# Optimization experiments

Measured on AMD Instinct MI355X. Metric: run time of the kernel, lower is better.

## Reference

```python
import jax, jax.numpy as jnp
import numpy as np

B = 200
SIZES = [65536, 16384, 4096, 1024, 256, 64]
DEG = 9
LOG_SIGMA = -1000.0  # weight log-sigma init (-1000) -> sigma = exp(-1000) == 0 in fp32, deterministic sample w = mu
P_DROP = 0.1
BN_EPS = 1e-5


def setup_inputs() -> dict:
    key = jax.random.key(0)
    ks = iter(jax.random.split(key, 64))
    d = {"x": jax.random.normal(next(ks), (B, SIZES[0], 3), jnp.float32)}
    din = 3
    for l in range(5):
        nin, nout = SIZES[l], SIZES[l + 1]
        E = nout * DEG
        d[f"src{l+1}"] = jax.random.randint(next(ks), (E,), 0, nin, dtype=jnp.int32)
        d[f"dst{l+1}"] = jnp.sort(jax.random.randint(next(ks), (E,), 0, nout, dtype=jnp.int32))
        d[f"w{l+1}"] = 0.1 * jax.random.normal(next(ks), (E, din, 1), jnp.float32)
        d[f"b{l+1}"] = 0.01 * jax.random.normal(next(ks), (nout, 1), jnp.float32)
        if l < 4:
            d[f"gamma{l+1}"] = jnp.ones((nout,), jnp.float32)
            d[f"beta{l+1}"] = jnp.zeros((nout,), jnp.float32)
        din = 1
    return d


def _pool(h, src, dst, w_mu, bias, n_out):
    # Bayesian sparse pooler: w = mu + exp(LOG_SIGMA)*eps == mu (sigma underflows to 0 in fp32)
    msgs = jnp.einsum('bed,edo->beo', h[:, src], w_mu)  # (B, E, dout) gathered weighted messages
    out = jnp.zeros((h.shape[0], n_out, w_mu.shape[2]), h.dtype).at[:, dst].add(msgs) + bias
    kl = jnp.sum(0.5 * (w_mu * w_mu - 1.0) - LOG_SIGMA)  # KL(N(mu, sig^2) || N(0, 1)) per weight, summed
    return out, kl


def _bn(h, gamma, beta):
    # training-mode BatchNorm1d over (B, C, 1): batch stats per channel (biased var, as torch)
    m = h.mean(axis=0, keepdims=True)
    v = h.var(axis=0, keepdims=True)
    hn = (h - m) * jax.lax.rsqrt(v + BN_EPS)
    return hn * gamma[None, :, None] + beta[None, :, None]


def _dropout(h, k):
    keep = jax.random.bernoulli(k, 1.0 - P_DROP, h.shape)
    return jnp.where(keep, h / (1.0 - P_DROP), jnp.zeros((), h.dtype))


def reference(x, src1, dst1, w1, b1, gamma1, beta1, src2, dst2, w2, b2, gamma2, beta2, src3, dst3, w3, b3, gamma3, beta3, src4, dst4, w4, b4, gamma4, beta4, src5, dst5, w5, b5):
    dkeys = jax.random.split(jax.random.key(42), 4)
    layers = [
        (src1, dst1, w1, b1, gamma1, beta1),
        (src2, dst2, w2, b2, gamma2, beta2),
        (src3, dst3, w3, b3, gamma3, beta3),
        (src4, dst4, w4, b4, gamma4, beta4),
    ]
    h = x
    kl_tot = jnp.float32(0.0)
    for l, (s, dd, w, b, g, bt) in enumerate(layers):
        h, kl = _pool(h, s, dd, w, b, SIZES[l + 1])
        kl_tot = kl_tot + kl
        h = _dropout(jax.nn.relu(_bn(h, g, bt)), dkeys[l])
    h, kl = _pool(h, src5, dst5, w5, b5, SIZES[5])
    kl_tot = kl_tot + kl
    return h[..., 0], kl_tot  # (B, 64), scalar KL
```

## Files before the change

kernel.cpp:

```cpp
#include <hip/hip_runtime.h>
#include <hip/hip_fp16.h>
#include <stdint.h>

#define B_    200
#define N0    65536
#define COLS  (N0 * 3)
#define JT    64
#define TPAD2 228

__device__ static inline unsigned short f2h(float f) {
  __half h = __float2half(f);
  return *reinterpret_cast<unsigned short*>(&h);
}
__device__ static inline float h2f(unsigned short u) {
  __half h = *reinterpret_cast<__half*>(&u);
  return __half2float(h);
}

__host__ __device__ static inline void tf2x32(uint32_t k0, uint32_t k1,
                                              uint32_t x0, uint32_t x1,
                                              uint32_t& o0, uint32_t& o1) {
  const uint32_t ks2 = k0 ^ k1 ^ 0x1BD11BDAu;
  x0 += k0; x1 += k1;
#define TF_R(r) { x0 += x1; x1 = (x1 << (r)) | (x1 >> (32 - (r))); x1 ^= x0; }
  TF_R(13) TF_R(15) TF_R(26) TF_R(6)   x0 += k1;  x1 += ks2 + 1u;
  TF_R(17) TF_R(29) TF_R(16) TF_R(24)  x0 += ks2; x1 += k0  + 2u;
  TF_R(13) TF_R(15) TF_R(26) TF_R(6)   x0 += k0;  x1 += k1  + 3u;
  TF_R(17) TF_R(29) TF_R(16) TF_R(24)  x0 += k1;  x1 += ks2 + 4u;
  TF_R(13) TF_R(15) TF_R(26) TF_R(6)   x0 += ks2; x1 += k0  + 5u;
#undef TF_R
  o0 = x0; o1 = x1;
}

__device__ static inline float drop_mask_apply(float hn, uint32_t b, uint32_t c,
                                               uint32_t nout, uint32_t k0, uint32_t k1) {
  uint32_t o0, o1;
  tf2x32(k0, k1, 0u, b * nout + c, o0, o1);
  uint32_t bits = o0 ^ o1;
  float u = __uint_as_float((bits >> 9) | 0x3f800000u) - 1.0f;
  return (u < 0.9f) ? hn * (1.0f / 0.9f) : 0.0f;
}

__global__ void build_rp_all(const int* __restrict__ dst0, const int* __restrict__ dst1,
                             const int* __restrict__ dst2, const int* __restrict__ dst3,
                             const int* __restrict__ dst4,
                             int* rp0, int* rp1, int* rp2, int* rp3, int* rp4,
                             float* kl) {
  int tid = blockIdx.x * blockDim.x + threadIdx.x;
  if (tid == 0) *kl = 0.f;
  if (tid >= 21829) return;
  const int starts[6] = {0, 16385, 20482, 21507, 21764, 21829};
  const int EDGa[5]   = {147456, 36864, 9216, 2304, 576};
  const int* dsts[5]  = {dst0, dst1, dst2, dst3, dst4};
  int* rps[5]         = {rp0, rp1, rp2, rp3, rp4};
  int l = 0;
  while (tid >= starts[l + 1]) ++l;
  int c = tid - starts[l];
  const int* dst = dsts[l];
  int lo = 0, hi = EDGa[l];
  while (lo < hi) { int mid = (lo + hi) >> 1; if (dst[mid] < c) lo = mid + 1; else hi = mid; }
  rps[l][c] = lo;
}

__global__ __launch_bounds__(256) void kl_all_kernel(
    const float* __restrict__ w0, const float* __restrict__ w1,
    const float* __restrict__ w2, const float* __restrict__ w3,
    const float* __restrict__ w4, float* __restrict__ out) {
  __shared__ float red[256];
  const float* ws[5] = {w0, w1, w2, w3, w4};
  const int    ns[5] = {442368, 36864, 9216, 2304, 576};
  int stride = gridDim.x * blockDim.x;
  int tid0 = blockIdx.x * blockDim.x + threadIdx.x;
  float s = 0.f;
#pragma unroll
  for (int l = 0; l < 5; ++l) {
    const float* w = ws[l];
    int n = ns[l];
    for (int i = tid0; i < n; i += stride) {
      float v = w[i];
      s += fmaf(0.5f * v, v, 999.5f);
    }
  }
  red[threadIdx.x] = s;
  __syncthreads();
  for (int st = 128; st > 0; st >>= 1) {
    if (threadIdx.x < st) red[threadIdx.x] += red[threadIdx.x + st];
    __syncthreads();
  }
  if (threadIdx.x == 0) atomicAdd(out, red[0]);
}

__global__ __launch_bounds__(512, 4) void transpose_rows_kernel(
    const float* __restrict__ x, unsigned short* __restrict__ xT2) {
  __shared__ unsigned short tile[JT * TPAD2];
  const int t  = threadIdx.x;
  const int j0 = blockIdx.x * JT;
  const int tx = t & 15;
  const int bl = t >> 4;

  const float* xp = x + j0 + (tx << 2);
  float4 v[7];
#pragma unroll
  for (int p = 0; p < 7; ++p) {
    int b = bl + (p << 5);
    b = b < B_ ? b : B_ - 1;
    v[p] = *(const float4*)(xp + (size_t)b * COLS);
  }
  __builtin_amdgcn_sched_barrier(0);
#pragma unroll
  for (int p = 0; p < 7; ++p) {
    int b = bl + (p << 5);
    if (b < B_) {
      int base = (tx << 2) * TPAD2 + b;
      tile[base            ] = f2h(v[p].x);
      tile[base +     TPAD2] = f2h(v[p].y);
      tile[base + 2 * TPAD2] = f2h(v[p].z);
      tile[base + 3 * TPAD2] = f2h(v[p].w);
    }
  }
  __syncthreads();
#pragma unroll
  for (int q = 0; q < 7; ++q) {
    unsigned idx = (unsigned)t + ((unsigned)q << 9);
    if (idx < 3200u) {
      unsigned row = idx / 50u;
      unsigned g   = idx - row * 50u;
      uint2 o = *(const uint2*)&tile[row * TPAD2 + (g << 2)];
      *(uint2*)(xT2 + (size_t)(j0 + row) * B_ + (g << 2)) = o;
    }
  }
}

__global__ __launch_bounds__(256) void pool1_bn_wave(
    const unsigned short* __restrict__ xT2, const int* __restrict__ src,
    const float* __restrict__ w, const float* __restrict__ bias,
    const int* __restrict__ rp, const float* __restrict__ gamma,
    const float* __restrict__ beta, unsigned short* __restrict__ out,
    uint32_t k0, uint32_t k1) {
  const int l   = threadIdx.x & 63;
  const int c   = (blockIdx.x << 2) + (threadIdx.x >> 6);
  const int l2  = l << 1;
  const bool hi = (l < 36);
  const int lm2 = (hi ? l2 : 70) + 128;

  float a00 = 0.f, a01 = 0.f, a10 = 0.f, a11 = 0.f;
  const int e0 = rp[c], e1 = rp[c + 1];
  int e = e0;
#define P1_EDGE(EE)                                                          \
  {                                                                          \
    const unsigned short* base = xT2 + (size_t)src[EE] * (3 * B_);           \
    float w0 = w[3 * (EE)], w1 = w[3 * (EE) + 1], w2 = w[3 * (EE) + 2];      \
    uint32_t p0 = *(const uint32_t*)(base +           l2);                   \
    uint32_t p1 = *(const uint32_t*)(base +     B_ +  l2);                   \
    uint32_t p2 = *(const uint32_t*)(base + 2 * B_ +  l2);                   \
    uint32_t q0 = *(const uint32_t*)(base +           lm2);                  \
    uint32_t q1 = *(const uint32_t*)(base +     B_ +  lm2);                  \
    uint32_t q2 = *(const uint32_t*)(base + 2 * B_ +  lm2);                  \
    a00 = fmaf(h2f((unsigned short)p0), w0, a00);                            \
    a01 = fmaf(h2f((unsigned short)(p0 >> 16)), w0, a01);                    \
    a00 = fmaf(h2f((unsigned short)p1), w1, a00);                            \
    a01 = fmaf(h2f((unsigned short)(p1 >> 16)), w1, a01);                    \
    a00 = fmaf(h2f((unsigned short)p2), w2, a00);                            \
    a01 = fmaf(h2f((unsigned short)(p2 >> 16)), w2, a01);                    \
    a10 = fmaf(h2f((unsigned short)q0), w0, a10);                            \
    a11 = fmaf(h2f((unsigned short)(q0 >> 16)), w0, a11);                    \
    a10 = fmaf(h2f((unsigned short)q1), w1, a10);                            \
    a11 = fmaf(h2f((unsigned short)(q1 >> 16)), w1, a11);                    \
    a10 = fmaf(h2f((unsigned short)q2), w2, a10);                            \
    a11 = fmaf(h2f((unsigned short)(q2 >> 16)), w2, a11);                    \
  }
  for (; e + 2 <= e1; e += 2) { P1_EDGE(e) P1_EDGE(e + 1) }
  for (; e < e1; ++e) { P1_EDGE(e) }
#undef P1_EDGE
  const float bi = bias[c];
  a00 += bi; a01 += bi; a10 += bi; a11 += bi;

  float sv = a00 + a01 + (hi ? a10 + a11 : 0.f);
  float qv = a00 * a00 + a01 * a01 + (hi ? a10 * a10 + a11 * a11 : 0.f);
#pragma unroll
  for (int off = 32; off; off >>= 1) {
    sv += __shfl_xor(sv, off);
    qv += __shfl_xor(qv, off);
  }
  const float m   = sv * (1.f / 200.f);
  const float var = fmaf(qv, 1.f / 200.f, -m * m);
  const float scale = gamma[c] * rsqrtf(var + 1e-5f);
  const float shift = fmaf(-m, scale, beta[c]);

  float r0 = drop_mask_apply(fmaxf(fmaf(a00, scale, shift), 0.f), (uint32_t)l2,      (uint32_t)c, 16384u, k0, k1);
  float r1 = drop_mask_apply(fmaxf(fmaf(a01, scale, shift), 0.f), (uint32_t)l2 + 1u, (uint32_t)c, 16384u, k0, k1);
  *(uint32_t*)(out + (size_t)c * B_ + l2) = (uint32_t)f2h(r0) | ((uint32_t)f2h(r1) << 16);
  if (hi) {
    float r2 = drop_mask_apply(fmaxf(fmaf(a10, scale, shift), 0.f), (uint32_t)(128 + l2), (uint32_t)c, 16384u, k0, k1);
    float r3 = drop_mask_apply(fmaxf(fmaf(a11, scale, shift), 0.f), (uint32_t)(129 + l2), (uint32_t)c, 16384u, k0, k1);
    *(uint32_t*)(out + (size_t)c * B_ + 128 + l2) = (uint32_t)f2h(r2) | ((uint32_t)f2h(r3) << 16);
  }
}

__global__ __launch_bounds__(256) void pooln_wave(
    const unsigned short* __restrict__ hin, const int* __restrict__ src,
    const float* __restrict__ w, const float* __restrict__ bias,
    const int* __restrict__ rp, const float* __restrict__ gamma,
    const float* __restrict__ beta, void* __restrict__ outv,
    int nout, int has_bn, uint32_t k0, uint32_t k1) {
  const int l   = threadIdx.x & 63;
  const int c   = (blockIdx.x << 2) + (threadIdx.x >> 6);
  const int l2  = l << 1;
  const bool hi = (l < 36);
  const int lm2 = (hi ? l2 : 70) + 128;

  float a00 = 0.f, a01 = 0.f, a10 = 0.f, a11 = 0.f;
  const int e0 = rp[c], e1 = rp[c + 1];
  int e = e0;
#define PN_EDGE(EE)                                                          \
  {                                                                          \
    const unsigned short* base = hin + (size_t)src[EE] * B_;                 \
    float we = w[EE];                                                        \
    uint32_t p0 = *(const uint32_t*)(base + l2);                             \
    uint32_t q0 = *(const uint32_t*)(base + lm2);                            \
    a00 = fmaf(h2f((unsigned short)p0), we, a00);                            \
    a01 = fmaf(h2f((unsigned short)(p0 >> 16)), we, a01);                    \
    a10 = fmaf(h2f((unsigned short)q0), we, a10);                            \
    a11 = fmaf(h2f((unsigned short)(q0 >> 16)), we, a11);                    \
  }
  for (; e + 2 <= e1; e += 2) { PN_EDGE(e) PN_EDGE(e + 1) }
  for (; e < e1; ++e) { PN_EDGE(e) }
#undef PN_EDGE
  const float bi = bias[c];
  a00 += bi; a01 += bi; a10 += bi; a11 += bi;

  if (has_bn) {
    float sv = a00 + a01 + (hi ? a10 + a11 : 0.f);
    float qv = a00 * a00 + a01 * a01 + (hi ? a10 * a10 + a11 * a11 : 0.f);
#pragma unroll
    for (int off = 32; off; off >>= 1) {
      sv += __shfl_xor(sv, off);
      qv += __shfl_xor(qv, off);
    }
    const float m   = sv * (1.f / 200.f);
    const float var = fmaf(qv, 1.f / 200.f, -m * m);
    const float scale = gamma[c] * rsqrtf(var + 1e-5f);
    const float shift = fmaf(-m, scale, beta[c]);
    unsigned short* out = (unsigned short*)outv;
    uint32_t no = (uint32_t)nout;
    float r0 = drop_mask_apply(fmaxf(fmaf(a00, scale, shift), 0.f), (uint32_t)l2,      (uint32_t)c, no, k0, k1);
    float r1 = drop_mask_apply(fmaxf(fmaf(a01, scale, shift), 0.f), (uint32_t)l2 + 1u, (uint32_t)c, no, k0, k1);
    *(uint32_t*)(out + (size_t)c * B_ + l2) = (uint32_t)f2h(r0) | ((uint32_t)f2h(r1) << 16);
    if (hi) {
      float r2 = drop_mask_apply(fmaxf(fmaf(a10, scale, shift), 0.f), (uint32_t)(128 + l2), (uint32_t)c, no, k0, k1);
      float r3 = drop_mask_apply(fmaxf(fmaf(a11, scale, shift), 0.f), (uint32_t)(129 + l2), (uint32_t)c, no, k0, k1);
      *(uint32_t*)(out + (size_t)c * B_ + 128 + l2) = (uint32_t)f2h(r2) | ((uint32_t)f2h(r3) << 16);
    }
  } else {
    float* out = (float*)outv;
    out[(size_t)l2 * 64 + c]       = a00;
    out[(size_t)(l2 + 1) * 64 + c] = a01;
    if (hi) {
      out[(size_t)(128 + l2) * 64 + c] = a10;
      out[(size_t)(129 + l2) * 64 + c] = a11;
    }
  }
}

extern "C" void kernel_launch(void* const* d_in, const int* in_sizes, int n_in,
                              void* d_out, int out_size, void* d_ws, size_t ws_size,
                              hipStream_t stream) {
  (void)in_sizes; (void)n_in; (void)out_size; (void)ws_size;
  const float* x = (const float*)d_in[0];
  const int*   src[5]; const int* dst[5];
  const float* w[5];   const float* bias[5];
  const float* gamma[4]; const float* beta[4];
  int idx = 1;
  for (int l = 0; l < 5; ++l) {
    src[l]  = (const int*)d_in[idx++];
    dst[l]  = (const int*)d_in[idx++];
    w[l]    = (const float*)d_in[idx++];
    bias[l] = (const float*)d_in[idx++];
    if (l < 4) { gamma[l] = (const float*)d_in[idx++]; beta[l] = (const float*)d_in[idx++]; }
  }
  static const int NOUT[5] = {16384, 4096, 1024, 256, 64};

  uint32_t dk0[4], dk1[4];
  for (uint32_t i = 0; i < 4; ++i) tf2x32(0u, 42u, 0u, i, dk0[i], dk1[i]);

  char* ws = (char*)d_ws;
  size_t off = 0;
  auto carve = [&](size_t bytes) -> void* {
    void* p = ws + off;
    off = (off + bytes + 255) & ~(size_t)255;
    return p;
  };
  int* rp[5];
  for (int l = 0; l < 5; ++l) rp[l] = (int*)carve((size_t)(NOUT[l] + 1) * sizeof(int));
  unsigned short* h1 = (unsigned short*)carve((size_t)16384 * B_ * 2);
  unsigned short* h2 = (unsigned short*)carve((size_t)4096 * B_ * 2);
  unsigned short* h3 = (unsigned short*)carve((size_t)1024 * B_ * 2);
  unsigned short* h4 = (unsigned short*)carve((size_t)256 * B_ * 2);
  unsigned short* xT2 = (unsigned short*)carve((size_t)COLS * B_ * 2);

  float* kl = (float*)d_out + 12800;

  build_rp_all<<<(21829 + 255) / 256, 256, 0, stream>>>(
      dst[0], dst[1], dst[2], dst[3], dst[4],
      rp[0], rp[1], rp[2], rp[3], rp[4], kl);

  kl_all_kernel<<<256, 256, 0, stream>>>(w[0], w[1], w[2], w[3], w[4], kl);

  transpose_rows_kernel<<<COLS / JT, 512, 0, stream>>>(x, xT2);

  pool1_bn_wave<<<16384 / 4, 256, 0, stream>>>(
      xT2, src[0], w[0], bias[0], rp[0], gamma[0], beta[0], h1,
      dk0[0], dk1[0]);

  pooln_wave<<<4096 / 4, 256, 0, stream>>>(
      h1, src[1], w[1], bias[1], rp[1], gamma[1], beta[1], h2, 4096, 1,
      dk0[1], dk1[1]);
  pooln_wave<<<1024 / 4, 256, 0, stream>>>(
      h2, src[2], w[2], bias[2], rp[2], gamma[2], beta[2], h3, 1024, 1,
      dk0[2], dk1[2]);
  pooln_wave<<<256 / 4, 256, 0, stream>>>(
      h3, src[3], w[3], bias[3], rp[3], gamma[3], beta[3], h4, 256, 1,
      dk0[3], dk1[3]);
  pooln_wave<<<64 / 4, 256, 0, stream>>>(
      h4, src[4], w[4], bias[4], rp[4], nullptr, nullptr, (float*)d_out, 64, 0,
      0u, 0u);
}
```

Baseline: 114.3 us.

## Split each channel's edges across two waves and widen per-lane batch loads

Each output channel is now handled by two wavefronts that take alternating edges. Their partial sums are combined through shared memory before the BatchNorm and dropout epilogue. Each lane now loads four contiguous fp16 batch values as one 8-byte load instead of two scattered 4-byte loads, and only 50 of 64 lanes stay active. The transpose kernel also swizzles its block index so neighbouring blocks touch spread-out column ranges. The aim is more memory-level parallelism for the gather-bound pooling layers, at the cost of a block-wide barrier and idle lanes.

New measurement: 111.0 us, median of 2. -2.9%, faster.

```diff
diff --git a/kernel.cpp b/kernel.cpp
--- a/kernel.cpp
+++ b/kernel.cpp
@@ -94,7 +94,10 @@
     const float* __restrict__ x, unsigned short* __restrict__ xT2) {
   __shared__ unsigned short tile[JT * TPAD2];
   const int t  = threadIdx.x;
-  const int j0 = blockIdx.x * JT;
+  const int nb = COLS / JT;
+  const int bid = (int)blockIdx.x;
+  const int sb  = (bid & 7) * (nb >> 3) + (bid >> 3);
+  const int j0 = sb * JT;
   const int tx = t & 15;
   const int bl = t >> 4;
 
@@ -137,46 +140,56 @@
     const int* __restrict__ rp, const float* __restrict__ gamma,
     const float* __restrict__ beta, unsigned short* __restrict__ out,
     uint32_t k0, uint32_t k1) {
-  const int l   = threadIdx.x & 63;
-  const int c   = (blockIdx.x << 2) + (threadIdx.x >> 6);
-  const int l2  = l << 1;
-  const bool hi = (l < 36);
-  const int lm2 = (hi ? l2 : 70) + 128;
-
-  float a00 = 0.f, a01 = 0.f, a10 = 0.f, a11 = 0.f;
-  const int e0 = rp[c], e1 = rp[c + 1];
-  int e = e0;
+  __shared__ float part[2][64][4];
+  const int l    = threadIdx.x & 63;
+  const int wid  = threadIdx.x >> 6;
+  const int chl  = wid & 1;
+  const int half = wid >> 1;
+  const int c    = ((int)blockIdx.x << 1) + chl;
+  const bool act = (l < 50);
+  const int b4   = (act ? l : 0) << 2;
+
+  float a0 = 0.f, a1 = 0.f, a2 = 0.f, a3 = 0.f;
+  const int e1 = rp[c + 1];
+  int e = rp[c] + half;
 #define P1_EDGE(EE)                                                          \
   {                                                                          \
-    const unsigned short* base = xT2 + (size_t)src[EE] * (3 * B_);           \
+    const unsigned short* base = xT2 + (size_t)src[EE] * (3 * B_) + b4;      \
     float w0 = w[3 * (EE)], w1 = w[3 * (EE) + 1], w2 = w[3 * (EE) + 2];      \
-    uint32_t p0 = *(const uint32_t*)(base +           l2);                   \
-    uint32_t p1 = *(const uint32_t*)(base +     B_ +  l2);                   \
-    uint32_t p2 = *(const uint32_t*)(base + 2 * B_ +  l2);                   \
-    uint32_t q0 = *(const uint32_t*)(base +           lm2);                  \
-    uint32_t q1 = *(const uint32_t*)(base +     B_ +  lm2);                  \
-    uint32_t q2 = *(const uint32_t*)(base + 2 * B_ +  lm2);                  \
-    a00 = fmaf(h2f((unsigned short)p0), w0, a00);                            \
-    a01 = fmaf(h2f((unsigned short)(p0 >> 16)), w0, a01);                    \
-    a00 = fmaf(h2f((unsigned short)p1), w1, a00);                            \
-    a01 = fmaf(h2f((unsigned short)(p1 >> 16)), w1, a01);                    \
-    a00 = fmaf(h2f((unsigned short)p2), w2, a00);                            \
-    a01 = fmaf(h2f((unsigned short)(p2 >> 16)), w2, a01);                    \
-    a10 = fmaf(h2f((unsigned short)q0), w0, a10);                            \
-    a11 = fmaf(h2f((unsigned short)(q0 >> 16)), w0, a11);                    \
-    a10 = fmaf(h2f((unsigned short)q1), w1, a10);                            \
-    a11 = fmaf(h2f((unsigned short)(q1 >> 16)), w1, a11);                    \
-    a10 = fmaf(h2f((unsigned short)q2), w2, a10);                            \
-    a11 = fmaf(h2f((unsigned short)(q2 >> 16)), w2, a11);                    \
-  }
-  for (; e + 2 <= e1; e += 2) { P1_EDGE(e) P1_EDGE(e + 1) }
-  for (; e < e1; ++e) { P1_EDGE(e) }
+    uint2 p0 = *(const uint2*)(base);                                        \
+    uint2 p1 = *(const uint2*)(base + B_);                                   \
+    uint2 p2 = *(const uint2*)(base + 2 * B_);                               \
+    a0 = fmaf(h2f((unsigned short)p0.x), w0, a0);                            \
+    a1 = fmaf(h2f((unsigned short)(p0.x >> 16)), w0, a1);                    \
+    a2 = fmaf(h2f((unsigned short)p0.y), w0, a2);                            \
+    a3 = fmaf(h2f((unsigned short)(p0.y >> 16)), w0, a3);                    \
+    a0 = fmaf(h2f((unsigned short)p1.x), w1, a0);                            \
+    a1 = fmaf(h2f((unsigned short)(p1.x >> 16)), w1, a1);                    \
+    a2 = fmaf(h2f((unsigned short)p1.y), w1, a2);                            \
+    a3 = fmaf(h2f((unsigned short)(p1.y >> 16)), w1, a3);                    \
+    a0 = fmaf(h2f((unsigned short)p2.x), w2, a0);                            \
+    a1 = fmaf(h2f((unsigned short)(p2.x >> 16)), w2, a1);                    \
+    a2 = fmaf(h2f((unsigned short)p2.y), w2, a2);                            \
+    a3 = fmaf(h2f((unsigned short)(p2.y >> 16)), w2, a3);                    \
+  }
+  for (; e + 2 < e1; e += 4) { P1_EDGE(e) P1_EDGE(e + 2) }
+  for (; e < e1; e += 2) { P1_EDGE(e) }
 #undef P1_EDGE
+
+  if (half == 1) {
+    part[chl][l][0] = a0; part[chl][l][1] = a1;
+    part[chl][l][2] = a2; part[chl][l][3] = a3;
+  }
+  __syncthreads();
+  if (half == 1) return;
+  a0 += part[chl][l][0]; a1 += part[chl][l][1];
+  a2 += part[chl][l][2]; a3 += part[chl][l][3];
   const float bi = bias[c];
-  a00 += bi; a01 += bi; a10 += bi; a11 += bi;
-
-  float sv = a00 + a01 + (hi ? a10 + a11 : 0.f);
-  float qv = a00 * a00 + a01 * a01 + (hi ? a10 * a10 + a11 * a11 : 0.f);
+  a0 += bi; a1 += bi; a2 += bi; a3 += bi;
+  if (!act) { a0 = a1 = a2 = a3 = 0.f; }
+
+  float sv = a0 + a1 + a2 + a3;
+  float qv = a0 * a0 + a1 * a1 + a2 * a2 + a3 * a3;
 #pragma unroll
   for (int off = 32; off; off >>= 1) {
     sv += __shfl_xor(sv, off);
@@ -187,13 +200,15 @@
   const float scale = gamma[c] * rsqrtf(var + 1e-5f);
   const float shift = fmaf(-m, scale, beta[c]);
 
-  float r0 = drop_mask_apply(fmaxf(fmaf(a00, scale, shift), 0.f), (uint32_t)l2,      (uint32_t)c, 16384u, k0, k1);
-  float r1 = drop_mask_apply(fmaxf(fmaf(a01, scale, shift), 0.f), (uint32_t)l2 + 1u, (uint32_t)c, 16384u, k0, k1);
-  *(uint32_t*)(out + (size_t)c * B_ + l2) = (uint32_t)f2h(r0) | ((uint32_t)f2h(r1) << 16);
-  if (hi) {
-    float r2 = drop_mask_apply(fmaxf(fmaf(a10, scale, shift), 0.f), (uint32_t)(128 + l2), (uint32_t)c, 16384u, k0, k1);
-    float r3 = drop_mask_apply(fmaxf(fmaf(a11, scale, shift), 0.f), (uint32_t)(129 + l2), (uint32_t)c, 16384u, k0, k1);
-    *(uint32_t*)(out + (size_t)c * B_ + 128 + l2) = (uint32_t)f2h(r2) | ((uint32_t)f2h(r3) << 16);
+  if (act) {
+    float r0 = drop_mask_apply(fmaxf(fmaf(a0, scale, shift), 0.f), (uint32_t)b4,      (uint32_t)c, 16384u, k0, k1);
+    float r1 = drop_mask_apply(fmaxf(fmaf(a1, scale, shift), 0.f), (uint32_t)b4 + 1u, (uint32_t)c, 16384u, k0, k1);
+    float r2 = drop_mask_apply(fmaxf(fmaf(a2, scale, shift), 0.f), (uint32_t)b4 + 2u, (uint32_t)c, 16384u, k0, k1);
+    float r3 = drop_mask_apply(fmaxf(fmaf(a3, scale, shift), 0.f), (uint32_t)b4 + 3u, (uint32_t)c, 16384u, k0, k1);
+    uint2 pk;
+    pk.x = (uint32_t)f2h(r0) | ((uint32_t)f2h(r1) << 16);
+    pk.y = (uint32_t)f2h(r2) | ((uint32_t)f2h(r3) << 16);
+    *(uint2*)(out + (size_t)c * B_ + b4) = pk;
   }
 }
 
@@ -203,35 +218,47 @@
     const int* __restrict__ rp, const float* __restrict__ gamma,
     const float* __restrict__ beta, void* __restrict__ outv,
     int nout, int has_bn, uint32_t k0, uint32_t k1) {
-  const int l   = threadIdx.x & 63;
-  const int c   = (blockIdx.x << 2) + (threadIdx.x >> 6);
-  const int l2  = l << 1;
-  const bool hi = (l < 36);
-  const int lm2 = (hi ? l2 : 70) + 128;
-
-  float a00 = 0.f, a01 = 0.f, a10 = 0.f, a11 = 0.f;
-  const int e0 = rp[c], e1 = rp[c + 1];
-  int e = e0;
+  __shared__ float part[2][64][4];
+  const int l    = threadIdx.x & 63;
+  const int wid  = threadIdx.x >> 6;
+  const int chl  = wid & 1;
+  const int half = wid >> 1;
+  const int c    = ((int)blockIdx.x << 1) + chl;
+  const bool act = (l < 50);
+  const int b4   = (act ? l : 0) << 2;
+
+  float a0 = 0.f, a1 = 0.f, a2 = 0.f, a3 = 0.f;
+  const int e1 = rp[c + 1];
+  int e = rp[c] + half;
 #define PN_EDGE(EE)                                                          \
   {                                                                          \
-    const unsigned short* base = hin + (size_t)src[EE] * B_;                 \
+    const unsigned short* base = hin + (size_t)src[EE] * B_ + b4;            \
     float we = w[EE];                                                        \
-    uint32_t p0 = *(const uint32_t*)(base + l2);                             \
-    uint32_t q0 = *(const uint32_t*)(base + lm2);                            \
-    a00 = fmaf(h2f((unsigned short)p0), we, a00);                            \
-    a01 = fmaf(h2f((unsigned short)(p0 >> 16)), we, a01);                    \
-    a10 = fmaf(h2f((unsigned short)q0), we, a10);                            \
-    a11 = fmaf(h2f((unsigned short)(q0 >> 16)), we, a11);                    \
-  }
-  for (; e + 2 <= e1; e += 2) { PN_EDGE(e) PN_EDGE(e + 1) }
-  for (; e < e1; ++e) { PN_EDGE(e) }
+    uint2 p0 = *(const uint2*)(base);                                        \
+    a0 = fmaf(h2f((unsigned short)p0.x), we, a0);                            \
+    a1 = fmaf(h2f((unsigned short)(p0.x >> 16)), we, a1);                    \
+    a2 = fmaf(h2f((unsigned short)p0.y), we, a2);                            \
+    a3 = fmaf(h2f((unsigned short)(p0.y >> 16)), we, a3);                    \
+  }
+  for (; e + 2 < e1; e += 4) { PN_EDGE(e) PN_EDGE(e + 2) }
+  for (; e < e1; e += 2) { PN_EDGE(e) }
 #undef PN_EDGE
+
+  if (half == 1) {
+    part[chl][l][0] = a0; part[chl][l][1] = a1;
+    part[chl][l][2] = a2; part[chl][l][3] = a3;
+  }
+  __syncthreads();
+  if (half == 1) return;
+  a0 += part[chl][l][0]; a1 += part[chl][l][1];
+  a2 += part[chl][l][2]; a3 += part[chl][l][3];
   const float bi = bias[c];
-  a00 += bi; a01 += bi; a10 += bi; a11 += bi;
+  a0 += bi; a1 += bi; a2 += bi; a3 += bi;
 
   if (has_bn) {
-    float sv = a00 + a01 + (hi ? a10 + a11 : 0.f);
-    float qv = a00 * a00 + a01 * a01 + (hi ? a10 * a10 + a11 * a11 : 0.f);
+    if (!act) { a0 = a1 = a2 = a3 = 0.f; }
+    float sv = a0 + a1 + a2 + a3;
+    float qv = a0 * a0 + a1 * a1 + a2 * a2 + a3 * a3;
 #pragma unroll
     for (int off = 32; off; off >>= 1) {
       sv += __shfl_xor(sv, off);
@@ -241,24 +268,24 @@
     const float var = fmaf(qv, 1.f / 200.f, -m * m);
     const float scale = gamma[c] * rsqrtf(var + 1e-5f);
     const float shift = fmaf(-m, scale, beta[c]);
-    unsigned short* out = (unsigned short*)outv;
-    uint32_t no = (uint32_t)nout;
-    float r0 = drop_mask_apply(fmaxf(fmaf(a00, scale, shift), 0.f), (uint32_t)l2,      (uint32_t)c, no, k0, k1);
-    float r1 = drop_mask_apply(fmaxf(fmaf(a01, scale, shift), 0.f), (uint32_t)l2 + 1u, (uint32_t)c, no, k0, k1);
-    *(uint32_t*)(out + (size_t)c * B_ + l2) = (uint32_t)f2h(r0) | ((uint32_t)f2h(r1) << 16);
-    if (hi) {
-      float r2 = drop_mask_apply(fmaxf(fmaf(a10, scale, shift), 0.f), (uint32_t)(128 + l2), (uint32_t)c, no, k0, k1);
-      float r3 = drop_mask_apply(fmaxf(fmaf(a11, scale, shift), 0.f), (uint32_t)(129 + l2), (uint32_t)c, no, k0, k1);
-      *(uint32_t*)(out + (size_t)c * B_ + 128 + l2) = (uint32_t)f2h(r2) | ((uint32_t)f2h(r3) << 16);
-    }
-  } else {
+    if (act) {
+      unsigned short* out = (unsigned short*)outv;
+      uint32_t no = (uint32_t)nout;
+      float r0 = drop_mask_apply(fmaxf(fmaf(a0, scale, shift), 0.f), (uint32_t)b4,      (uint32_t)c, no, k0, k1);
+      float r1 = drop_mask_apply(fmaxf(fmaf(a1, scale, shift), 0.f), (uint32_t)b4 + 1u, (uint32_t)c, no, k0, k1);
+      float r2 = drop_mask_apply(fmaxf(fmaf(a2, scale, shift), 0.f), (uint32_t)b4 + 2u, (uint32_t)c, no, k0, k1);
+      float r3 = drop_mask_apply(fmaxf(fmaf(a3, scale, shift), 0.f), (uint32_t)b4 + 3u, (uint32_t)c, no, k0, k1);
+      uint2 pk;
+      pk.x = (uint32_t)f2h(r0) | ((uint32_t)f2h(r1) << 16);
+      pk.y = (uint32_t)f2h(r2) | ((uint32_t)f2h(r3) << 16);
+      *(uint2*)(out + (size_t)c * B_ + b4) = pk;
+    }
+  } else if (act) {
     float* out = (float*)outv;
-    out[(size_t)l2 * 64 + c]       = a00;
-    out[(size_t)(l2 + 1) * 64 + c] = a01;
-    if (hi) {
-      out[(size_t)(128 + l2) * 64 + c] = a10;
-      out[(size_t)(129 + l2) * 64 + c] = a11;
-    }
+    out[(size_t)(b4    ) * 64 + c] = a0;
+    out[(size_t)(b4 + 1) * 64 + c] = a1;
+    out[(size_t)(b4 + 2) * 64 + c] = a2;
+    out[(size_t)(b4 + 3) * 64 + c] = a3;
   }
 }
 
@@ -308,20 +335,20 @@
 
   transpose_rows_kernel<<<COLS / JT, 512, 0, stream>>>(x, xT2);
 
-  pool1_bn_wave<<<16384 / 4, 256, 0, stream>>>(
+  pool1_bn_wave<<<16384 / 2, 256, 0, stream>>>(
       xT2, src[0], w[0], bias[0], rp[0], gamma[0], beta[0], h1,
       dk0[0], dk1[0]);
 
-  pooln_wave<<<4096 / 4, 256, 0, stream>>>(
+  pooln_wave<<<4096 / 2, 256, 0, stream>>>(
       h1, src[1], w[1], bias[1], rp[1], gamma[1], beta[1], h2, 4096, 1,
       dk0[1], dk1[1]);
-  pooln_wave<<<1024 / 4, 256, 0, stream>>>(
+  pooln_wave<<<1024 / 2, 256, 0, stream>>>(
       h2, src[2], w[2], bias[2], rp[2], gamma[2], beta[2], h3, 1024, 1,
       dk0[2], dk1[2]);
-  pooln_wave<<<256 / 4, 256, 0, stream>>>(
+  pooln_wave<<<256 / 2, 256, 0, stream>>>(
       h3, src[3], w[3], bias[3], rp[3], gamma[3], beta[3], h4, 256, 1,
       dk0[3], dk1[3]);
-  pooln_wave<<<64 / 4, 256, 0, stream>>>(
+  pooln_wave<<<64 / 2, 256, 0, stream>>>(
       h4, src[4], w[4], bias[4], rp[4], nullptr, nullptr, (float*)d_out, 64, 0,
       0u, 0u);
 }
```
